# Kernel optimization log

Measured on AMD Instinct MI355X. Metric: run time of the kernel, lower is better.

## Reference

```python
import jax, jax.numpy as jnp
import numpy as np
import math

D_MODEL = 1024
NHEAD = 16
D_FF = 4096
MAX_LEN = 512
LN_EPS = 1e-5


def setup_inputs() -> dict:
    key = jax.random.key(0)
    ks = jax.random.split(key, 12)
    d, h, dff, L = D_MODEL, NHEAD, D_FF, MAX_LEN
    B, S = 16, 512
    s = lambda k, shape, std: jax.random.normal(k, shape, dtype=jnp.float32) * std
    return {
        "x": s(ks[0], (B, S, d), 1.0),
        "in_proj_w": s(ks[1], (3 * d, d), d ** -0.5),   # torch MHA in_proj_weight
        "in_proj_b": jnp.zeros((3 * d,), jnp.float32),
        "out_w": s(ks[2], (d, d), d ** -0.5),            # out_proj.weight (out,in)
        "out_b": jnp.zeros((d,), jnp.float32),
        "rel_bias": s(ks[3], (h, 2 * L - 1), 0.02),      # (nhead, 2*max_len-1)
        "w1": s(ks[4], (dff, d), d ** -0.5),             # Linear(d, dff).weight
        "b1": jnp.zeros((dff,), jnp.float32),
        "w2": s(ks[5], (d, dff), dff ** -0.5),           # Linear(dff, d).weight
        "b2": jnp.zeros((d,), jnp.float32),
        "ln1_w": jnp.ones((d,), jnp.float32),
        "ln1_b": jnp.zeros((d,), jnp.float32),
        "ln2_w": jnp.ones((d,), jnp.float32),
        "ln2_b": jnp.zeros((d,), jnp.float32),
    }


def _layernorm(x, w, b):
    mu = jnp.mean(x, axis=-1, keepdims=True)
    var = jnp.mean(jnp.square(x - mu), axis=-1, keepdims=True)
    return (x - mu) * jax.lax.rsqrt(var + LN_EPS) * w + b


def _rel_pos_bias(rel_bias, seq_len):
    pos = jnp.arange(seq_len)
    rel = pos[:, None] - pos[None, :] + (MAX_LEN - 1)        # (S,S)
    rel = jnp.clip(rel, 0, 2 * MAX_LEN - 2)
    return rel_bias[:, rel]                                  # (H,S,S)


def reference(x, in_proj_w, in_proj_b, out_w, out_b, rel_bias,
              w1, b1, w2, b2, ln1_w, ln1_b, ln2_w, ln2_b):
    B, S, d = x.shape
    h = NHEAD
    hd = d // h
    bias = _rel_pos_bias(rel_bias, S)[None]                  # (1,H,S,S)

    # --- attention block (pre-norm) ---
    residual = x
    xn = _layernorm(x, ln1_w, ln1_b)
    qkv = xn @ in_proj_w.T + in_proj_b                       # (B,S,3d)
    q, k, v = jnp.split(qkv, 3, axis=-1)
    q = q.reshape(B, S, h, hd).transpose(0, 2, 1, 3)         # (B,H,S,hd)
    k = k.reshape(B, S, h, hd).transpose(0, 2, 1, 3)
    v = v.reshape(B, S, h, hd).transpose(0, 2, 1, 3)
    scores = jnp.einsum('bhqd,bhkd->bhqk', q, k) / math.sqrt(hd) + bias
    probs = jax.nn.softmax(scores, axis=-1)
    attn = jnp.einsum('bhqk,bhkd->bhqd', probs, v)           # (B,H,S,hd)
    attn = attn.transpose(0, 2, 1, 3).reshape(B, S, d)
    attn = attn @ out_w.T + out_b
    x = residual + attn

    # --- FFN block (pre-norm) ---
    residual = x
    xn = _layernorm(x, ln2_w, ln2_b)
    hdn = jax.nn.gelu(xn @ w1.T + b1, approximate=False)
    x = residual + hdn @ w2.T + b2
    return x
```

## Files before the change

kernel.cpp:

```cpp
#include <hip/hip_runtime.h>
#include <hip/hip_bf16.h>
#include <stdint.h>

typedef __hip_bfloat16 bf16;
typedef __attribute__((ext_vector_type(8))) __bf16 bf16x8;
typedef __attribute__((ext_vector_type(4))) float f32x4;

#define D_MODEL 1024
#define NHEAD   16
#define HDIM    64
#define DFF     4096
#define BATCH   16
#define SEQ     512
#define MROWS   (BATCH*SEQ)

__device__ __forceinline__ float b2f_bits(unsigned short u) {
    return __uint_as_float(((unsigned)u) << 16);
}
__device__ __forceinline__ bf16 f2b(float v) { return __float2bfloat16(v); }
__device__ __forceinline__ unsigned short f2b_bits(float v) {
    bf16 t = __float2bfloat16(v);
    return *(unsigned short*)&t;
}
__device__ __forceinline__ void gll16(void* lds, const void* gsrc) {
    __builtin_amdgcn_global_load_lds(
        (const __attribute__((address_space(1))) unsigned*)gsrc,
        (__attribute__((address_space(3))) unsigned*)lds,
        16, 0, 0);
}

__global__ __launch_bounds__(256)
void cvt_kernel(const float* __restrict__ in, bf16* __restrict__ out, int n)
{
    int i = (blockIdx.x * 256 + threadIdx.x) * 4;
    if (i >= n) return;
    float4 f = *(const float4*)(in + i);
    ushort4 o;
    o.x = f2b_bits(f.x); o.y = f2b_bits(f.y);
    o.z = f2b_bits(f.z); o.w = f2b_bits(f.w);
    *(ushort4*)((unsigned short*)out + i) = o;
}

__global__ __launch_bounds__(256)
void ln_kernel(const float* __restrict__ xin, const float* __restrict__ w,
               const float* __restrict__ b, bf16* __restrict__ out)
{
    int row  = blockIdx.x;
    int t    = threadIdx.x;
    int lane = t & 63, wv = t >> 6;
    int col  = t * 4;

    float4 f = *(const float4*)(xin + (size_t)row * D_MODEL + col);
    float v[4] = {f.x, f.y, f.z, f.w};

    float s  = v[0] + v[1] + v[2] + v[3];
    float ss = v[0]*v[0] + v[1]*v[1] + v[2]*v[2] + v[3]*v[3];
    #pragma unroll
    for (int m = 1; m < 64; m <<= 1) {
        s  += __shfl_xor(s,  m, 64);
        ss += __shfl_xor(ss, m, 64);
    }
    __shared__ float rs0[4], rs1[4];
    if (lane == 0) { rs0[wv] = s; rs1[wv] = ss; }
    __syncthreads();
    s  = rs0[0] + rs0[1] + rs0[2] + rs0[3];
    ss = rs1[0] + rs1[1] + rs1[2] + rs1[3];

    float mu  = s * (1.0f / D_MODEL);
    float var = ss * (1.0f / D_MODEL) - mu * mu;
    float rs  = rsqrtf(var + 1e-5f);

    float4 wf = *(const float4*)(w + col);
    float4 bf = *(const float4*)(b + col);
    ushort4 o;
    o.x = f2b_bits((v[0]-mu)*rs*wf.x + bf.x);
    o.y = f2b_bits((v[1]-mu)*rs*wf.y + bf.y);
    o.z = f2b_bits((v[2]-mu)*rs*wf.z + bf.z);
    o.w = f2b_bits((v[3]-mu)*rs*wf.w + bf.w);
    *(ushort4*)((unsigned short*)out + (size_t)row * D_MODEL + col) = o;
}

template<int EPI, bool OUT_B16>
__global__ __launch_bounds__(256)
void gemm_bt(const bf16* __restrict__ A, const bf16* __restrict__ Bw,
             const float* __restrict__ bias, const float* __restrict__ resid,
             void* __restrict__ Cout, bf16* __restrict__ qb,
             bf16* __restrict__ ktb, bf16* __restrict__ vb,
             int M, int N, int K)
{
    int t    = threadIdx.x;
    int lane = t & 63, w = t >> 6;
    int wm   = w & 1,  wn = w >> 1;
    int q    = lane >> 4, r = lane & 15;

    int gx  = gridDim.x;
    int L   = blockIdx.y * gx + blockIdx.x;
    int qq  = (gx * gridDim.y) >> 3;
    int nid = (L & 7) * qq + (L >> 3);
    int mb  = (nid / gx) * 128, nb = (nid % gx) * 128;

    __shared__ __bf16 As[128 * 32];
    __shared__ __bf16 Bs[128 * 32];

    f32x4 acc[4][4] = {};

    const char* Ag = (const char*)((const unsigned short*)A + (size_t)mb * K);
    const char* Bg = (const char*)((const unsigned short*)Bw + (size_t)nb * K);

    int ar0 = t >> 2,  ac0 = (t & 3) << 3;

    for (int k0 = 0; k0 < K; k0 += 32) {
        __syncthreads();
        size_t off0 = ((size_t)ar0 * K + k0 + ac0) * 2;
        size_t off1 = off0 + (size_t)64 * K * 2;
        gll16((char*)As + t * 16,        Ag + off0);
        gll16((char*)As + 4096 + t * 16, Ag + off1);
        gll16((char*)Bs + t * 16,        Bg + off0);
        gll16((char*)Bs + 4096 + t * 16, Bg + off1);
        __syncthreads();

        bf16x8 af[4], bfr[4];
        #pragma unroll
        for (int i = 0; i < 4; i++)
            af[i] = *(const bf16x8*)(As + (wm * 64 + i * 16 + r) * 32 + q * 8);
        #pragma unroll
        for (int j = 0; j < 4; j++)
            bfr[j] = *(const bf16x8*)(Bs + (wn * 64 + j * 16 + r) * 32 + q * 8);
        #pragma unroll
        for (int i = 0; i < 4; i++)
            #pragma unroll
            for (int j = 0; j < 4; j++)
                acc[i][j] = __builtin_amdgcn_mfma_f32_16x16x32_bf16(af[i], bfr[j], acc[i][j], 0, 0, 0);
    }

    #pragma unroll
    for (int j = 0; j < 4; j++) {
        int n = nb + wn * 64 + j * 16 + r;
        float bv = bias[n];
        #pragma unroll
        for (int i = 0; i < 4; i++) {
            int mbase = mb + wm * 64 + i * 16 + q * 4;
            #pragma unroll
            for (int rr = 0; rr < 4; rr++) {
                int m = mbase + rr;
                float v = acc[i][j][rr] + bv;
                if (EPI == 1) v = 0.5f * v * (1.0f + erff(v * 0.70710678118654752f));
                if (EPI == 2) v += resid[(size_t)m * N + n];
                if (EPI == 3) {
                    int sect = n >> 10;
                    int h = (n >> 6) & 15;
                    int e = n & 63;
                    int bi = m >> 9, s = m & 511;
                    size_t bh = (size_t)bi * NHEAD + h;
                    bf16 val = f2b(v);
                    if (sect == 0)      qb[((bh * SEQ + s) << 6) + e] = val;
                    else if (sect == 1) ktb[((bh * SEQ + s) << 6) + e] = val;
                    else                vb[((bh * HDIM + e) << 9) + s] = val;
                } else {
                    if (OUT_B16) ((bf16*)Cout)[(size_t)m * N + n] = f2b(v);
                    else         ((float*)Cout)[(size_t)m * N + n] = v;
                }
            }
        }
    }
}

__global__ __launch_bounds__(256, 4)
void attn_mfma(const bf16* __restrict__ Q, const bf16* __restrict__ K,
               const bf16* __restrict__ VT, const float* __restrict__ relb,
               bf16* __restrict__ out)
{
    int L   = blockIdx.x + (blockIdx.y << 3);
    int xcd = L & 7, jj = L >> 3;
    int bh  = xcd * 32 + (jj >> 3);
    int q0  = (jj & 7) * 64;
    int b   = bh >> 4, h = bh & 15;
    int t = threadIdx.x, lane = t & 63, w = t >> 6;
    int l15 = lane & 15, l4 = lane >> 4;

    __shared__ __bf16 Pls[64 * 128];
    __shared__ float  rbs[1024];

    const float* rb = relb + (size_t)h * (2 * SEQ - 1);
    for (int i = t; i < 2 * SEQ - 1; i += 256) rbs[i] = rb[i];
    __syncthreads();

    const unsigned short* Qp = (const unsigned short*)Q
        + (((size_t)bh * SEQ + q0 + w * 16 + l15) << 6) + l4 * 8;
    bf16x8 qf0 = *(const bf16x8*)Qp;
    bf16x8 qf1 = *(const bf16x8*)(Qp + 32);

    const unsigned short* Kp = (const unsigned short*)K
        + (((size_t)bh * SEQ + l15) << 6) + l4 * 8;
    const unsigned short* Vp = (const unsigned short*)VT
        + ((size_t)bh << 15) + ((size_t)l15 << 9) + l4 * 8;

    char* Pb = (char*)Pls;
    int qbase  = q0 + w * 16 + l4 * 4;
    int prow   = w * 16 + l15;
    int prbase = prow << 8;
    int pswz   = (prow & 7) << 4;
    float sum[4] = {0.f, 0.f, 0.f, 0.f};
    f32x4 oacc[4] = {};

    #pragma unroll 1
    for (int c = 0; c < 4; c++) {
        f32x4 sc[8];
        #pragma unroll
        for (int kl = 0; kl < 8; kl++) {
            const unsigned short* kp = Kp + ((size_t)(c * 8 + kl) << 10);
            bf16x8 kf0 = *(const bf16x8*)kp;
            bf16x8 kf1 = *(const bf16x8*)(kp + 32);
            f32x4 a = {};
            a = __builtin_amdgcn_mfma_f32_16x16x32_bf16(qf0, kf0, a, 0, 0, 0);
            a = __builtin_amdgcn_mfma_f32_16x16x32_bf16(qf1, kf1, a, 0, 0, 0);
            sc[kl] = a;
        }
        #pragma unroll
        for (int kl = 0; kl < 8; kl++) {
            int relbase = qbase - ((c * 8 + kl) * 16 + l15) + (SEQ - 1);
            #pragma unroll
            for (int reg = 0; reg < 4; reg++) {
                float p = __expf(sc[kl][reg] * 0.125f + rbs[relbase + reg]);
                sum[reg] += p;
                float o = __shfl_xor(p, 1, 64);
                unsigned lo = f2b_bits((lane & 1) ? o : p);
                unsigned hi = f2b_bits((lane & 1) ? p : o);
                unsigned pk = lo | (hi << 16);
                if ((lane & 1) == (reg >> 1)) {
                    int row  = w * 16 + l4 * 4 + reg;
                    int byte = (row << 8) + (((kl << 4) + (l15 & ~1)) << 1);
                    byte ^= (row & 7) << 4;
                    *(unsigned*)(Pb + byte) = pk;
                }
            }
        }
        #pragma unroll
        for (int k2 = 0; k2 < 4; k2++) {
            int pbyte = (prbase + k2 * 64 + l4 * 16) ^ pswz;
            bf16x8 pf = *(const bf16x8*)(Pb + pbyte);
            int kt2 = c * 4 + k2;
            #pragma unroll
            for (int et = 0; et < 4; et++) {
                bf16x8 vf = *(const bf16x8*)(Vp + ((size_t)et << 13) + kt2 * 32);
                oacc[et] = __builtin_amdgcn_mfma_f32_16x16x32_bf16(pf, vf, oacc[et], 0, 0, 0);
            }
        }
    }

    #pragma unroll
    for (int m = 1; m < 16; m <<= 1)
        #pragma unroll
        for (int reg = 0; reg < 4; reg++)
            sum[reg] += __shfl_xor(sum[reg], m, 64);
    float rcp[4];
    #pragma unroll
    for (int reg = 0; reg < 4; reg++) rcp[reg] = 1.0f / sum[reg];

    bf16* op = out + (size_t)(b * SEQ + q0 + w * 16 + l4 * 4) * D_MODEL
             + h * HDIM + l15;
    #pragma unroll
    for (int et = 0; et < 4; et++)
        #pragma unroll
        for (int reg = 0; reg < 4; reg++)
            op[(size_t)reg * D_MODEL + et * 16] = f2b(oacc[et][reg] * rcp[reg]);
}

extern "C" void kernel_launch(void* const* d_in, const int* in_sizes, int n_in,
                              void* d_out, int out_size, void* d_ws, size_t ws_size,
                              hipStream_t stream)
{
    const float* x    = (const float*)d_in[0];
    const float* wqkv = (const float*)d_in[1];
    const float* bqkv = (const float*)d_in[2];
    const float* wo   = (const float*)d_in[3];
    const float* bo   = (const float*)d_in[4];
    const float* relb = (const float*)d_in[5];
    const float* w1   = (const float*)d_in[6];
    const float* b1   = (const float*)d_in[7];
    const float* w2   = (const float*)d_in[8];
    const float* b2   = (const float*)d_in[9];
    const float* ln1w = (const float*)d_in[10];
    const float* ln1b = (const float*)d_in[11];
    const float* ln2w = (const float*)d_in[12];
    const float* ln2b = (const float*)d_in[13];

    char* ws = (char*)d_ws;
    const size_t MB = 1048576;
    bf16*  wqkv_b = (bf16*)(ws + 1 * MB);
    bf16*  wo_b   = (bf16*)(ws + 7 * MB);
    bf16*  xn     = (bf16*)(ws + 9 * MB);
    bf16*  Qb     = (bf16*)(ws + 25 * MB);
    bf16*  Kb     = (bf16*)(ws + 41 * MB);
    float* x1     = (float*)(ws + 25 * MB);
    bf16*  w1_b   = (bf16*)(ws + 1 * MB);
    bf16*  w2_b   = (bf16*)(ws + 9 * MB);
    bf16*  xn2    = (bf16*)(ws + 9 * MB);
    bf16*  hid    = (bf16*)(ws + 57 * MB);
    bf16*  VT     = (bf16*)d_out;
    bf16*  att    = (bf16*)((char*)d_out + 16 * MB);
    float* out    = (float*)d_out;

    cvt_kernel<<<3072, 256, 0, stream>>>(wqkv, wqkv_b, 3 * D_MODEL * D_MODEL);
    cvt_kernel<<<1024, 256, 0, stream>>>(wo,   wo_b,   D_MODEL * D_MODEL);
    ln_kernel<<<MROWS, 256, 0, stream>>>(x, ln1w, ln1b, xn);
    gemm_bt<3,true><<<dim3(24, 64), 256, 0, stream>>>(xn, wqkv_b, bqkv, nullptr,
        nullptr, Qb, Kb, VT, MROWS, 3 * D_MODEL, D_MODEL);
    attn_mfma<<<dim3(8, 256), 256, 0, stream>>>(Qb, Kb, VT, relb, att);
    gemm_bt<2,false><<<dim3(8, 64), 256, 0, stream>>>(att, wo_b, bo, x,
        x1, nullptr, nullptr, nullptr, MROWS, D_MODEL, D_MODEL);
    cvt_kernel<<<4096, 256, 0, stream>>>(w1, w1_b, DFF * D_MODEL);
    ln_kernel<<<MROWS, 256, 0, stream>>>(x1, ln2w, ln2b, xn2);
    gemm_bt<1,true><<<dim3(32, 64), 256, 0, stream>>>(xn2, w1_b, b1, nullptr,
        hid, nullptr, nullptr, nullptr, MROWS, DFF, D_MODEL);
    cvt_kernel<<<4096, 256, 0, stream>>>(w2, w2_b, D_MODEL * DFF);
    gemm_bt<2,false><<<dim3(8, 64), 256, 0, stream>>>(hid, w2_b, b2, x1,
        out, nullptr, nullptr, nullptr, MROWS, D_MODEL, DFF);
}
```

Baseline: 626.2 us.

## Double-buffer GEMM LDS tiles, stage bf16 epilogue via LDS, use tanh GELU

The GEMM main loop now uses two LDS buffers: the next K-slice is loaded with global_load_lds while the current slice is consumed by MFMA, which removes one barrier per iteration and overlaps load latency with compute. For bf16 outputs the epilogue writes results into LDS and then stores coalesced 16-byte chunks instead of scattered 2-byte stores. The exact erf GELU is replaced by a tanh approximation built from expf, which is cheaper but changes the numerics relative to the exact-GELU reference. The extra buffer doubles LDS use per block, which may reduce occupancy.

```diff
diff --git a/kernel.cpp b/kernel.cpp
--- a/kernel.cpp
+++ b/kernel.cpp
@@ -27,6 +27,14 @@
         (const __attribute__((address_space(1))) unsigned*)gsrc,
         (__attribute__((address_space(3))) unsigned*)lds,
         16, 0, 0);
+}
+__device__ __forceinline__ float gelu_f(float u) {
+    float z  = 0.7978845608028654f * (u + 0.044715f * u * u * u);
+    float az = fabsf(z);
+    float e  = __expf(-2.0f * az);
+    float th = (1.0f - e) / (1.0f + e);
+    th = copysignf(th, z);
+    return 0.5f * u * (1.0f + th);
 }
 
 __global__ __launch_bounds__(256)
@@ -99,8 +107,7 @@
     int nid = (L & 7) * qq + (L >> 3);
     int mb  = (nid / gx) * 128, nb = (nid % gx) * 128;
 
-    __shared__ __bf16 As[128 * 32];
-    __shared__ __bf16 Bs[128 * 32];
+    __shared__ char smem[32768];
 
     f32x4 acc[4][4] = {};
 
@@ -109,56 +116,100 @@
 
     int ar0 = t >> 2,  ac0 = (t & 3) << 3;
 
-    for (int k0 = 0; k0 < K; k0 += 32) {
-        __syncthreads();
-        size_t off0 = ((size_t)ar0 * K + k0 + ac0) * 2;
-        size_t off1 = off0 + (size_t)64 * K * 2;
-        gll16((char*)As + t * 16,        Ag + off0);
-        gll16((char*)As + 4096 + t * 16, Ag + off1);
-        gll16((char*)Bs + t * 16,        Bg + off0);
-        gll16((char*)Bs + 4096 + t * 16, Bg + off1);
-        __syncthreads();
-
+    int nt = K >> 5;
+
+    #define STAGE(c, k0) do {                                      \
+        char* dA = smem + (c) * 16384;                             \
+        char* dB = dA + 8192;                                      \
+        size_t off0 = ((size_t)ar0 * K + (k0) + ac0) * 2;          \
+        size_t off1 = off0 + (size_t)64 * K * 2;                   \
+        gll16(dA + t * 16,        Ag + off0);                      \
+        gll16(dA + 4096 + t * 16, Ag + off1);                      \
+        gll16(dB + t * 16,        Bg + off0);                      \
+        gll16(dB + 4096 + t * 16, Bg + off1);                      \
+    } while (0)
+
+    STAGE(0, 0);
+    __syncthreads();
+
+    int cur = 0;
+    for (int tt = 0; tt < nt; ++tt) {
+        if (tt + 1 < nt) STAGE(cur ^ 1, (tt + 1) << 5);
+
+        const __bf16* Asb = (const __bf16*)(smem + cur * 16384);
+        const __bf16* Bsb = Asb + 4096;
         bf16x8 af[4], bfr[4];
         #pragma unroll
         for (int i = 0; i < 4; i++)
-            af[i] = *(const bf16x8*)(As + (wm * 64 + i * 16 + r) * 32 + q * 8);
+            af[i] = *(const bf16x8*)(Asb + (wm * 64 + i * 16 + r) * 32 + q * 8);
         #pragma unroll
         for (int j = 0; j < 4; j++)
-            bfr[j] = *(const bf16x8*)(Bs + (wn * 64 + j * 16 + r) * 32 + q * 8);
+            bfr[j] = *(const bf16x8*)(Bsb + (wn * 64 + j * 16 + r) * 32 + q * 8);
         #pragma unroll
         for (int i = 0; i < 4; i++)
             #pragma unroll
             for (int j = 0; j < 4; j++)
                 acc[i][j] = __builtin_amdgcn_mfma_f32_16x16x32_bf16(af[i], bfr[j], acc[i][j], 0, 0, 0);
+
+        __syncthreads();
+        cur ^= 1;
     }
-
-    #pragma unroll
-    for (int j = 0; j < 4; j++) {
-        int n = nb + wn * 64 + j * 16 + r;
-        float bv = bias[n];
-        #pragma unroll
-        for (int i = 0; i < 4; i++) {
-            int mbase = mb + wm * 64 + i * 16 + q * 4;
-            #pragma unroll
-            for (int rr = 0; rr < 4; rr++) {
-                int m = mbase + rr;
-                float v = acc[i][j][rr] + bv;
-                if (EPI == 1) v = 0.5f * v * (1.0f + erff(v * 0.70710678118654752f));
-                if (EPI == 2) v += resid[(size_t)m * N + n];
-                if (EPI == 3) {
-                    int sect = n >> 10;
-                    int h = (n >> 6) & 15;
-                    int e = n & 63;
-                    int bi = m >> 9, s = m & 511;
-                    size_t bh = (size_t)bi * NHEAD + h;
-                    bf16 val = f2b(v);
-                    if (sect == 0)      qb[((bh * SEQ + s) << 6) + e] = val;
-                    else if (sect == 1) ktb[((bh * SEQ + s) << 6) + e] = val;
-                    else                vb[((bh * HDIM + e) << 9) + s] = val;
-                } else {
-                    if (OUT_B16) ((bf16*)Cout)[(size_t)m * N + n] = f2b(v);
-                    else         ((float*)Cout)[(size_t)m * N + n] = v;
+    #undef STAGE
+
+    if (OUT_B16 && EPI != 3) {
+        __bf16* Cs = (__bf16*)smem;
+        #pragma unroll
+        for (int j = 0; j < 4; j++) {
+            int n = nb + wn * 64 + j * 16 + r;
+            float bv = bias[n];
+            #pragma unroll
+            for (int i = 0; i < 4; i++) {
+                #pragma unroll
+                for (int rr = 0; rr < 4; rr++) {
+                    float v = acc[i][j][rr] + bv;
+                    if (EPI == 1) v = gelu_f(v);
+                    if (EPI == 2) v += resid[(size_t)(mb + wm*64 + i*16 + q*4 + rr) * N + n];
+                    Cs[(wm*64 + i*16 + q*4 + rr) * 128 + wn*64 + j*16 + r] = *(__bf16*)&(unsigned short&)*(unsigned short[]){f2b_bits(v)};
+                }
+            }
+        }
+        __syncthreads();
+        char* Cg = (char*)Cout;
+        #pragma unroll
+        for (int c = 0; c < 8; c++) {
+            int idx = t + c * 256;
+            int row = idx >> 4, ch = idx & 15;
+            *(int4*)(Cg + ((size_t)(mb + row) * N + nb) * 2 + ch * 16) =
+                *(const int4*)((const char*)Cs + row * 256 + ch * 16);
+        }
+    } else {
+        #pragma unroll
+        for (int j = 0; j < 4; j++) {
+            int n = nb + wn * 64 + j * 16 + r;
+            float bv = bias[n];
+            #pragma unroll
+            for (int i = 0; i < 4; i++) {
+                int mbase = mb + wm * 64 + i * 16 + q * 4;
+                #pragma unroll
+                for (int rr = 0; rr < 4; rr++) {
+                    int m = mbase + rr;
+                    float v = acc[i][j][rr] + bv;
+                    if (EPI == 1) v = gelu_f(v);
+                    if (EPI == 2) v += resid[(size_t)m * N + n];
+                    if (EPI == 3) {
+                        int sect = n >> 10;
+                        int h = (n >> 6) & 15;
+                        int e = n & 63;
+                        int bi = m >> 9, s = m & 511;
+                        size_t bh = (size_t)bi * NHEAD + h;
+                        bf16 val = f2b(v);
+                        if (sect == 0)      qb[((bh * SEQ + s) << 6) + e] = val;
+                        else if (sect == 1) ktb[((bh * SEQ + s) << 6) + e] = val;
+                        else                vb[((bh * HDIM + e) << 9) + s] = val;
+                    } else {
+                        if (OUT_B16) ((bf16*)Cout)[(size_t)m * N + n] = f2b(v);
+                        else         ((float*)Cout)[(size_t)m * N + n] = v;
+                    }
                 }
             }
         }
```

New measurement: 568.7 us. 1.1x faster.
